# Kernel optimization log

Measured on AMD Instinct MI355X. Metric: run time of the kernel, lower is better.

The kernel has to match this reference:

```python
import jax, jax.numpy as jnp
import numpy as np
import math

N_HEADS = 16
DIM = 1024
D_HEAD = DIM // N_HEADS
BS, QLEN = 2, 2048


def setup_inputs() -> dict:
    key = jax.random.key(0)
    ks = jax.random.split(key, 10)
    s = 0.02
    return {
        "input": jax.random.normal(ks[0], (BS, QLEN, DIM), dtype=jnp.float32),
        "mask": jnp.ones((BS, QLEN), dtype=jnp.int32),
        "q_w": jax.random.normal(ks[1], (DIM, DIM), dtype=jnp.float32) * s,
        "q_b": jax.random.normal(ks[2], (DIM,), dtype=jnp.float32) * s,
        "k_w": jax.random.normal(ks[3], (DIM, DIM), dtype=jnp.float32) * s,
        "k_b": jax.random.normal(ks[4], (DIM,), dtype=jnp.float32) * s,
        "v_w": jax.random.normal(ks[5], (DIM, DIM), dtype=jnp.float32) * s,
        "v_b": jax.random.normal(ks[6], (DIM,), dtype=jnp.float32) * s,
        "o_w": jax.random.normal(ks[7], (DIM, DIM), dtype=jnp.float32) * s,
        "o_b": jax.random.normal(ks[8], (DIM,), dtype=jnp.float32) * s,
    }


def _shape(x, bs):
    # (bs, len, dim) -> (bs, heads, len, d_head)
    return x.reshape(bs, -1, N_HEADS, D_HEAD).transpose(0, 2, 1, 3)


def reference(input, mask, q_w, q_b, k_w, k_b, v_w, v_b, o_w, o_b):
    bs, qlen, dim = input.shape
    # projections (torch Linear: x @ W^T + b)
    q = _shape(input @ q_w.T + q_b, bs)
    k = _shape(input @ k_w.T + k_b, bs)
    v = _shape(input @ v_w.T + v_b, bs)
    q = q / math.sqrt(D_HEAD)
    # scores: (bs, heads, qlen, klen)
    scores = jnp.einsum("bhqd,bhkd->bhqk", q, k)
    pad = (mask == 0)[:, None, None, :]  # (bs,1,1,klen)
    scores = jnp.where(pad, -jnp.inf, scores)
    weights = jax.nn.softmax(scores.astype(jnp.float32), axis=-1).astype(scores.dtype)
    # dropout p=0.0 (eval) -> identity
    context = jnp.einsum("bhqk,bhkd->bhqd", weights, v)
    context = context.transpose(0, 2, 1, 3).reshape(bs, qlen, dim)
    return context @ o_w.T + o_b
```

## Files before the change

### kernel.cpp

```cpp
#include <hip/hip_runtime.h>


#define BS    2
#define QLEN  2048
#define DIM   1024
#define NH    16
#define DH    64
#define MTOK  (BS * QLEN)

#define QSCALE 0.18033688011112042f

typedef __attribute__((ext_vector_type(8))) short short8;
typedef __attribute__((ext_vector_type(4))) float float4_t;
typedef __attribute__((ext_vector_type(4))) int   int4_t;

__device__ __forceinline__ ushort f2bf(float f) {
    unsigned u = __float_as_uint(f);
    return (ushort)((u + 0x7fffu + ((u >> 16) & 1u)) >> 16);
}
__device__ __forceinline__ short8 pack8(float4 a0, float4 a1) {
    short8 r;
    r[0] = (short)f2bf(a0.x); r[1] = (short)f2bf(a0.y);
    r[2] = (short)f2bf(a0.z); r[3] = (short)f2bf(a0.w);
    r[4] = (short)f2bf(a1.x); r[5] = (short)f2bf(a1.y);
    r[6] = (short)f2bf(a1.z); r[7] = (short)f2bf(a1.w);
    return r;
}

__device__ __forceinline__ void glds16(const void* g, void* l) {
    __builtin_amdgcn_global_load_lds(
        (const __attribute__((address_space(1))) unsigned int*)g,
        (__attribute__((address_space(3))) unsigned int*)l, 16, 0, 0);
}

__global__ __launch_bounds__(256) void conv_all(
    const float* __restrict__ x,  const float* __restrict__ qw,
    const float* __restrict__ kw, const float* __restrict__ vw,
    const float* __restrict__ ow,
    ushort* __restrict__ Xbf, ushort* __restrict__ Wbf)
{
    const int blk = blockIdx.x;
    const float* s; ushort* d; size_t base;
    if (blk < 4096)      { s = x;  d = Xbf;             base = (size_t)blk * 1024; }
    else if (blk < 5120) { s = qw; d = Wbf;             base = (size_t)(blk - 4096) * 1024; }
    else if (blk < 6144) { s = kw; d = Wbf + 1048576;   base = (size_t)(blk - 5120) * 1024; }
    else if (blk < 7168) { s = vw; d = Wbf + 2097152;   base = (size_t)(blk - 6144) * 1024; }
    else                 { s = ow; d = Wbf + 3145728;   base = (size_t)(blk - 7168) * 1024; }
    const size_t i = base + threadIdx.x * 4;
    float4 v = *(const float4*)(s + i);
    ushort4 o;
    o.x = f2bf(v.x); o.y = f2bf(v.y); o.z = f2bf(v.z); o.w = f2bf(v.w);
    *(ushort4*)(d + i) = o;
}

__global__ __launch_bounds__(256) void transpose_v(
    const ushort* __restrict__ Vrow, ushort* __restrict__ Vt)
{
    __shared__ ushort T[64][72];
    const int tid  = threadIdx.x;
    const int tile = blockIdx.x;
    const int bh   = blockIdx.y;
    const int b = bh >> 4, h = bh & 15;

    #pragma unroll
    for (int rep = 0; rep < 2; ++rep) {
        int ch = tid + rep * 256;
        int tok = ch >> 3, seg = ch & 7;
        uint4 v = *(const uint4*)(Vrow + (size_t)(b * QLEN + tile * 64 + tok) * DIM
                                        + h * DH + seg * 8);
        *(uint4*)&T[tok][seg * 8] = v;
    }
    __syncthreads();
    #pragma unroll
    for (int rep = 0; rep < 2; ++rep) {
        int ch = tid + rep * 256;
        int dim = ch >> 3, tseg = ch & 7;
        ushort t0 = T[tseg * 8 + 0][dim], t1 = T[tseg * 8 + 1][dim];
        ushort t2 = T[tseg * 8 + 2][dim], t3 = T[tseg * 8 + 3][dim];
        ushort t4 = T[tseg * 8 + 4][dim], t5 = T[tseg * 8 + 5][dim];
        ushort t6 = T[tseg * 8 + 6][dim], t7 = T[tseg * 8 + 7][dim];
        uint4 o;
        o.x = (unsigned)t0 | ((unsigned)t1 << 16);
        o.y = (unsigned)t2 | ((unsigned)t3 << 16);
        o.z = (unsigned)t4 | ((unsigned)t5 << 16);
        o.w = (unsigned)t6 | ((unsigned)t7 << 16);
        *(uint4*)(Vt + (size_t)bh * DH * QLEN + (size_t)dim * QLEN
                      + tile * 64 + tseg * 8) = o;
    }
}

__global__ __launch_bounds__(256) void gemm_m97(
    const ushort* __restrict__ A, const ushort* __restrict__ Bw,
    const float* __restrict__ bias0, const float* __restrict__ bias1,
    const float* __restrict__ bias2,
    ushort* __restrict__ outQ, ushort* __restrict__ outK, ushort* __restrict__ outV,
    float* __restrict__ outF,
    int N, int K, int mode)
{
    __shared__ ushort As[128 * 32];
    __shared__ ushort Bs[128 * 32];
    const int tid  = threadIdx.x;
    const int w    = tid >> 6;
    const int lane = tid & 63;
    const int r15  = lane & 15;
    const int quad = lane >> 4;
    const int nblk = N >> 7;
    const int brow = blockIdx.x / nblk;
    const int bcol = blockIdx.x - brow * nblk;
    const int wrow = (w >> 1) * 64;
    const int wcol = (w & 1) * 64;

    float4_t acc[4][4];
    #pragma unroll
    for (int i = 0; i < 4; ++i)
        #pragma unroll
        for (int j = 0; j < 4; ++j)
            acc[i][j] = (float4_t){0.f, 0.f, 0.f, 0.f};

    int ch0 = w * 64 + lane;
    int ch1 = ch0 + 256;
    const int row0 = ch0 >> 2, s0 = ch0 & 3, gk0 = s0 ^ ((row0 >> 1) & 3);
    const int row1 = ch1 >> 2, s1 = ch1 & 3, gk1 = s1 ^ ((row1 >> 1) & 3);

    const ushort* ga0 = A + (size_t)(brow * 128 + row0) * K + gk0 * 8;
    const ushort* ga1 = A + (size_t)(brow * 128 + row1) * K + gk1 * 8;
    const ushort* gb0 = Bw + (size_t)(bcol * 128 + row0) * K + gk0 * 8;
    const ushort* gb1 = Bw + (size_t)(bcol * 128 + row1) * K + gk1 * 8;

    for (int k0 = 0; k0 < K; k0 += 32) {
        __syncthreads();
        glds16(ga0 + k0, As + ch0 * 8);
        glds16(ga1 + k0, As + ch1 * 8);
        glds16(gb0 + k0, Bs + ch0 * 8);
        glds16(gb1 + k0, Bs + ch1 * 8);
        __syncthreads();

        short8 af[4], bf[4];
        #pragma unroll
        for (int ms = 0; ms < 4; ++ms) {
            int row = wrow + ms * 16 + r15;
            int s = quad ^ ((row >> 1) & 3);
            af[ms] = *(const short8*)&As[row * 32 + s * 8];
        }
        #pragma unroll
        for (int ns = 0; ns < 4; ++ns) {
            int row = wcol + ns * 16 + r15;
            int s = quad ^ ((row >> 1) & 3);
            bf[ns] = *(const short8*)&Bs[row * 32 + s * 8];
        }
        #pragma unroll
        for (int ms = 0; ms < 4; ++ms)
            #pragma unroll
            for (int ns = 0; ns < 4; ++ns)
                acc[ms][ns] = __builtin_amdgcn_mfma_f32_16x16x32_bf16(
                    af[ms], bf[ns], acc[ms][ns], 0, 0, 0);
    }

    #pragma unroll
    for (int ms = 0; ms < 4; ++ms) {
        const int rowg = brow * 128 + wrow + ms * 16 + quad * 4;
        #pragma unroll
        for (int ns = 0; ns < 4; ++ns) {
            const int colg = bcol * 128 + wcol + ns * 16 + r15;
            if (mode == 0) {
                if (colg < 1024) {
                    const float bb = bias0[colg];
                    #pragma unroll
                    for (int r = 0; r < 4; ++r)
                        outQ[(size_t)(rowg + r) * 1024 + colg] =
                            f2bf((acc[ms][ns][r] + bb) * QSCALE);
                } else if (colg < 2048) {
                    const float bb = bias1[colg - 1024];
                    #pragma unroll
                    for (int r = 0; r < 4; ++r)
                        outK[(size_t)(rowg + r) * 1024 + (colg - 1024)] =
                            f2bf(acc[ms][ns][r] + bb);
                } else {
                    const float bb = bias2[colg - 2048];
                    #pragma unroll
                    for (int r = 0; r < 4; ++r)
                        outV[(size_t)(rowg + r) * 1024 + (colg - 2048)] =
                            f2bf(acc[ms][ns][r] + bb);
                }
            } else {
                const float bb = bias0[colg];
                #pragma unroll
                for (int r = 0; r < 4; ++r)
                    outF[(size_t)(rowg + r) * 1024 + colg] = acc[ms][ns][r] + bb;
            }
        }
    }
}

__global__ __launch_bounds__(256) void gemm_f32in_bf16out(
    const float* __restrict__ X, const float* __restrict__ W,
    const float* __restrict__ B, ushort* __restrict__ Out,
    int M, int N, int K, float scale)
{
    const int lane = threadIdx.x & 63;
    const int wid  = (blockIdx.x * blockDim.x + threadIdx.x) >> 6;
    const int tilesN = N >> 4;
    const int tm = wid / tilesN;
    const int tn = wid - tm * tilesN;
    const int r15  = lane & 15;
    const int quad = lane >> 4;

    const float* xp = X + (size_t)(tm * 16 + r15) * K + quad * 8;
    const float* wp = W + (size_t)(tn * 16 + r15) * K + quad * 8;

    float4_t acc = {0.f, 0.f, 0.f, 0.f};
    for (int k0 = 0; k0 < K; k0 += 32) {
        float4 a0 = *(const float4*)(xp + k0);
        float4 a1 = *(const float4*)(xp + k0 + 4);
        float4 b0 = *(const float4*)(wp + k0);
        float4 b1 = *(const float4*)(wp + k0 + 4);
        acc = __builtin_amdgcn_mfma_f32_16x16x32_bf16(pack8(a0, a1), pack8(b0, b1), acc, 0, 0, 0);
    }
    const int col  = tn * 16 + r15;
    const float bias = B[col];
    const int row0 = tm * 16 + quad * 4;
    #pragma unroll
    for (int r = 0; r < 4; ++r)
        Out[(size_t)(row0 + r) * N + col] = f2bf((acc[r] + bias) * scale);
}

__global__ __launch_bounds__(256) void gemm_bf16in_f32out(
    const ushort* __restrict__ X, const float* __restrict__ W,
    const float* __restrict__ B, float* __restrict__ Out,
    int M, int N, int K)
{
    const int lane = threadIdx.x & 63;
    const int wid  = (blockIdx.x * blockDim.x + threadIdx.x) >> 6;
    const int tilesN = N >> 4;
    const int tm = wid / tilesN;
    const int tn = wid - tm * tilesN;
    const int r15  = lane & 15;
    const int quad = lane >> 4;

    const ushort* xp = X + (size_t)(tm * 16 + r15) * K + quad * 8;
    const float*  wp = W + (size_t)(tn * 16 + r15) * K + quad * 8;

    float4_t acc = {0.f, 0.f, 0.f, 0.f};
    for (int k0 = 0; k0 < K; k0 += 32) {
        short8 a = *(const short8*)(xp + k0);
        float4 b0 = *(const float4*)(wp + k0);
        float4 b1 = *(const float4*)(wp + k0 + 4);
        acc = __builtin_amdgcn_mfma_f32_16x16x32_bf16(a, pack8(b0, b1), acc, 0, 0, 0);
    }
    const int col  = tn * 16 + r15;
    const float bias = B[col];
    const int row0 = tm * 16 + quad * 4;
    #pragma unroll
    for (int r = 0; r < 4; ++r)
        Out[(size_t)(row0 + r) * N + col] = acc[r] + bias;
}

__global__ __launch_bounds__(256) void flash_attn(
    const ushort* __restrict__ Qb, const ushort* __restrict__ Kb,
    const ushort* __restrict__ Vt, const int* __restrict__ mask,
    ushort* __restrict__ Cb)
{
    __shared__ __align__(16) ushort Ks[64][72];
    __shared__ __align__(16) ushort Vs[64][72];
    __shared__ __align__(16) float  Mb[QLEN];

    const int tid  = threadIdx.x;
    const int w    = tid >> 6;
    const int lane = tid & 63;
    const int r15  = lane & 15;
    const int quad = lane >> 4;
    const int bh = blockIdx.y;
    const int b = bh >> 4, h = bh & 15;

    {
        const int4* m4 = (const int4*)(mask + b * QLEN);
        #pragma unroll
        for (int rep = 0; rep < 2; ++rep) {
            const int idx = tid + rep * 256;
            int4 mv = m4[idx];
            float4 o;
            o.x = mv.x ? 0.f : -INFINITY;
            o.y = mv.y ? 0.f : -INFINITY;
            o.z = mv.z ? 0.f : -INFINITY;
            o.w = mv.w ? 0.f : -INFINITY;
            *(float4*)&Mb[idx * 4] = o;
        }
    }

    const int qbase = blockIdx.x * 128 + w * 32;
    const ushort* qp = Qb + (size_t)(b * QLEN + qbase + r15) * DIM + h * DH + quad * 8;
    short8 qf[2][2];
    qf[0][0] = *(const short8*)(qp);
    qf[0][1] = *(const short8*)(qp + 32);
    qf[1][0] = *(const short8*)(qp + 16 * DIM);
    qf[1][1] = *(const short8*)(qp + 16 * DIM + 32);

    const ushort* kg = Kb + (size_t)b * QLEN * DIM + h * DH;
    const ushort* vg = Vt + (size_t)bh * DH * QLEN;

    const int a0 = tid >> 3, seg = tid & 7;
    const int krow0 = (((a0 & 7) >> 2) << 4) + (((a0 >> 3) & 3) << 2) + (a0 & 3);

    float4_t o[2][4];
    #pragma unroll
    for (int rg = 0; rg < 2; ++rg)
        #pragma unroll
        for (int ds = 0; ds < 4; ++ds)
            o[rg][ds] = (float4_t){0.f, 0.f, 0.f, 0.f};
    float lp[2] = {0.f, 0.f};

    uint4 kr0, kr1, vr0, vr1;
    kr0 = *(const uint4*)(kg + (size_t)(a0     ) * DIM + seg * 8);
    kr1 = *(const uint4*)(kg + (size_t)(a0 + 32) * DIM + seg * 8);
    vr0 = *(const uint4*)(vg + (size_t)(a0     ) * QLEN + seg * 8);
    vr1 = *(const uint4*)(vg + (size_t)(a0 + 32) * QLEN + seg * 8);

    for (int kt = 0; kt < QLEN; kt += 64) {
        __syncthreads();
        *(uint4*)&Ks[krow0     ][seg * 8] = kr0;
        *(uint4*)&Ks[krow0 + 32][seg * 8] = kr1;
        *(uint4*)&Vs[a0        ][seg * 8] = vr0;
        *(uint4*)&Vs[a0 + 32   ][seg * 8] = vr1;
        __syncthreads();

        if (kt + 64 < QLEN) {
            kr0 = *(const uint4*)(kg + (size_t)(kt + 64 + a0     ) * DIM + seg * 8);
            kr1 = *(const uint4*)(kg + (size_t)(kt + 64 + a0 + 32) * DIM + seg * 8);
            vr0 = *(const uint4*)(vg + (size_t)(a0     ) * QLEN + kt + 64 + seg * 8);
            vr1 = *(const uint4*)(vg + (size_t)(a0 + 32) * QLEN + kt + 64 + seg * 8);
        }

        int pk[4][2][2];
        #pragma unroll
        for (int ks = 0; ks < 4; ++ks) {
            short8 kf0 = *(const short8*)&Ks[ks * 16 + r15][quad * 8];
            short8 kf1 = *(const short8*)&Ks[ks * 16 + r15][32 + quad * 8];
            const float4 mb = *(const float4*)&Mb[kt + ((ks >> 1) << 5)
                                                   + (quad << 3) + ((ks & 1) << 2)];
            #pragma unroll
            for (int rg = 0; rg < 2; ++rg) {
                float4_t s = {0.f, 0.f, 0.f, 0.f};
                s = __builtin_amdgcn_mfma_f32_16x16x32_bf16(kf0, qf[rg][0], s, 0, 0, 0);
                s = __builtin_amdgcn_mfma_f32_16x16x32_bf16(kf1, qf[rg][1], s, 0, 0, 0);
                unsigned u0 = __float_as_uint(exp2f(s[0] + mb.x));
                unsigned u1 = __float_as_uint(exp2f(s[1] + mb.y));
                unsigned u2 = __float_as_uint(exp2f(s[2] + mb.z));
                unsigned u3 = __float_as_uint(exp2f(s[3] + mb.w));
                lp[rg] += __uint_as_float(u0 & 0xffff0000u)
                        + __uint_as_float(u1 & 0xffff0000u)
                        + __uint_as_float(u2 & 0xffff0000u)
                        + __uint_as_float(u3 & 0xffff0000u);
                pk[ks][rg][0] = __builtin_amdgcn_perm(u1, u0, 0x07060302);
                pk[ks][rg][1] = __builtin_amdgcn_perm(u3, u2, 0x07060302);
            }
        }

        #pragma unroll
        for (int ck = 0; ck < 2; ++ck) {
            short8 vf[4];
            #pragma unroll
            for (int ds = 0; ds < 4; ++ds)
                vf[ds] = *(const short8*)&Vs[ds * 16 + r15][ck * 32 + quad * 8];
            #pragma unroll
            for (int rg = 0; rg < 2; ++rg) {
                int4_t pfi = { pk[2 * ck][rg][0], pk[2 * ck][rg][1],
                               pk[2 * ck + 1][rg][0], pk[2 * ck + 1][rg][1] };
                short8 pf = __builtin_bit_cast(short8, pfi);
                #pragma unroll
                for (int ds = 0; ds < 4; ++ds)
                    o[rg][ds] = __builtin_amdgcn_mfma_f32_16x16x32_bf16(
                        pf, vf[ds], o[rg][ds], 0, 0, 0);
            }
        }
    }

    #pragma unroll
    for (int rg = 0; rg < 2; ++rg) {
        float l = lp[rg];
        l += __shfl_xor(l, 16, 64);
        l += __shfl_xor(l, 32, 64);
        const float inv = 1.f / fmaxf(l, 1e-30f);
        #pragma unroll
        for (int r = 0; r < 4; ++r) {
            const float ir = __shfl(inv, quad * 4 + r, 64);
            const size_t rb = (size_t)(b * QLEN + qbase + rg * 16 + quad * 4 + r) * DIM
                              + h * DH;
            Cb[rb +  0 + r15] = f2bf(o[rg][0][r] * ir);
            Cb[rb + 16 + r15] = f2bf(o[rg][1][r] * ir);
            Cb[rb + 32 + r15] = f2bf(o[rg][2][r] * ir);
            Cb[rb + 48 + r15] = f2bf(o[rg][3][r] * ir);
        }
    }
}

extern "C" void kernel_launch(void* const* d_in, const int* in_sizes, int n_in,
                              void* d_out, int out_size, void* d_ws, size_t ws_size,
                              hipStream_t stream)
{
    const float* x    = (const float*)d_in[0];
    const int*   mask = (const int*)d_in[1];
    const float* q_w  = (const float*)d_in[2];
    const float* q_b  = (const float*)d_in[3];
    const float* k_w  = (const float*)d_in[4];
    const float* k_b  = (const float*)d_in[5];
    const float* v_w  = (const float*)d_in[6];
    const float* v_b  = (const float*)d_in[7];
    const float* o_w  = (const float*)d_in[8];
    const float* o_b  = (const float*)d_in[9];
    float* out = (float*)d_out;

    const size_t SEG = (size_t)MTOK * DIM;
    ushort* Qbf = (ushort*)d_out;
    ushort* Xbf = Qbf + SEG;
    ushort* Kb  = (ushort*)d_ws;
    ushort* Vrow = Kb + SEG;
    ushort* Cb   = Vrow;
    ushort* Vt  = Vrow + SEG;
    ushort* Wbf = Vt + SEG;

    const bool big = ws_size >= (size_t)32 * 1024 * 1024;

    if (big) {
        conv_all<<<8192, 256, 0, stream>>>(x, q_w, k_w, v_w, o_w, Xbf, Wbf);
        gemm_m97<<<(MTOK / 128) * (3072 / 128), 256, 0, stream>>>(
            Xbf, Wbf, q_b, k_b, v_b, Qbf, Kb, Vrow, nullptr, 3072, DIM, 0);
    } else {
        const int tiles   = (MTOK / 16) * (DIM / 16);
        const int gblocks = tiles / 4;
        gemm_f32in_bf16out<<<gblocks, 256, 0, stream>>>(x, q_w, q_b, Qbf, MTOK, DIM, DIM, QSCALE);
        gemm_f32in_bf16out<<<gblocks, 256, 0, stream>>>(x, k_w, k_b, Kb,  MTOK, DIM, DIM, 1.0f);
        gemm_f32in_bf16out<<<gblocks, 256, 0, stream>>>(x, v_w, v_b, Vrow, MTOK, DIM, DIM, 1.0f);
    }

    transpose_v<<<dim3(QLEN / 64, BS * NH), 256, 0, stream>>>(Vrow, Vt);

    flash_attn<<<dim3(QLEN / 128, BS * NH), 256, 0, stream>>>(Qbf, Kb, Vt, mask, Cb);

    if (big) {
        gemm_m97<<<(MTOK / 128) * (DIM / 128), 256, 0, stream>>>(
            Cb, Wbf + 3 * (size_t)(DIM * DIM), o_b, nullptr, nullptr,
            nullptr, nullptr, nullptr, out, DIM, DIM, 1);
    } else {
        const int tiles = (MTOK / 16) * (DIM / 16);
        gemm_bf16in_f32out<<<tiles / 4, 256, 0, stream>>>(Cb, o_w, o_b, out, MTOK, DIM, DIM);
    }
}
```

Measured before the change: 226.3 us.

## Double-buffer K/V LDS tiles with XOR swizzle and MFMA-based row sums

Replaces the single padded K/V shared tiles with double-buffered, XOR-swizzled unpadded tiles. The next tile is written to the alternate buffer after compute, so each iteration needs one barrier instead of two. The softmax denominator now comes from an extra MFMA against a ones vector instead of scalar adds and shuffles. exp2f is also replaced by the hardware exp2 intrinsic. This costs extra LDS for the second buffer and extra MFMA issue, and the swizzle indexing has to match the fragment layout exactly.

```diff
diff --git a/kernel.cpp b/kernel.cpp
--- a/kernel.cpp
+++ b/kernel.cpp
@@ -260,8 +260,8 @@
     const ushort* __restrict__ Vt, const int* __restrict__ mask,
     ushort* __restrict__ Cb)
 {
-    __shared__ __align__(16) ushort Ks[64][72];
-    __shared__ __align__(16) ushort Vs[64][72];
+    __shared__ __align__(16) ushort Ks[2][64][64];
+    __shared__ __align__(16) ushort Vs[2][64][64];
     __shared__ __align__(16) float  Mb[QLEN];
 
     const int tid  = threadIdx.x;
@@ -300,30 +300,37 @@
 
     const int a0 = tid >> 3, seg = tid & 7;
     const int krow0 = (((a0 & 7) >> 2) << 4) + (((a0 >> 3) & 3) << 2) + (a0 & 3);
+    const int sK = (seg ^ (krow0 & 7)) << 3;
+    const int sV = (seg ^ (a0 & 7)) << 3;
+    const int xq = (quad ^ (r15 & 7)) << 3;
 
     float4_t o[2][4];
-    #pragma unroll
-    for (int rg = 0; rg < 2; ++rg)
+    float4_t ol[2];
+    #pragma unroll
+    for (int rg = 0; rg < 2; ++rg) {
+        ol[rg] = (float4_t){0.f, 0.f, 0.f, 0.f};
         #pragma unroll
         for (int ds = 0; ds < 4; ++ds)
             o[rg][ds] = (float4_t){0.f, 0.f, 0.f, 0.f};
-    float lp[2] = {0.f, 0.f};
-
-    uint4 kr0, kr1, vr0, vr1;
-    kr0 = *(const uint4*)(kg + (size_t)(a0     ) * DIM + seg * 8);
-    kr1 = *(const uint4*)(kg + (size_t)(a0 + 32) * DIM + seg * 8);
-    vr0 = *(const uint4*)(vg + (size_t)(a0     ) * QLEN + seg * 8);
-    vr1 = *(const uint4*)(vg + (size_t)(a0 + 32) * QLEN + seg * 8);
-
+    }
+    short8 ones8;
+    #pragma unroll
+    for (int i = 0; i < 8; ++i) ones8[i] = (short)0x3F80;
+
+    uint4 kr0 = *(const uint4*)(kg + (size_t)(a0     ) * DIM + seg * 8);
+    uint4 kr1 = *(const uint4*)(kg + (size_t)(a0 + 32) * DIM + seg * 8);
+    uint4 vr0 = *(const uint4*)(vg + (size_t)(a0     ) * QLEN + seg * 8);
+    uint4 vr1 = *(const uint4*)(vg + (size_t)(a0 + 32) * QLEN + seg * 8);
+    *(uint4*)&Ks[0][krow0     ][sK] = kr0;
+    *(uint4*)&Ks[0][krow0 + 32][sK] = kr1;
+    *(uint4*)&Vs[0][a0        ][sV] = vr0;
+    *(uint4*)&Vs[0][a0 + 32   ][sV] = vr1;
+    __syncthreads();
+
+    int p = 0;
     for (int kt = 0; kt < QLEN; kt += 64) {
-        __syncthreads();
-        *(uint4*)&Ks[krow0     ][seg * 8] = kr0;
-        *(uint4*)&Ks[krow0 + 32][seg * 8] = kr1;
-        *(uint4*)&Vs[a0        ][seg * 8] = vr0;
-        *(uint4*)&Vs[a0 + 32   ][seg * 8] = vr1;
-        __syncthreads();
-
-        if (kt + 64 < QLEN) {
+        const bool more = (kt + 64 < QLEN);
+        if (more) {
             kr0 = *(const uint4*)(kg + (size_t)(kt + 64 + a0     ) * DIM + seg * 8);
             kr1 = *(const uint4*)(kg + (size_t)(kt + 64 + a0 + 32) * DIM + seg * 8);
             vr0 = *(const uint4*)(vg + (size_t)(a0     ) * QLEN + kt + 64 + seg * 8);
@@ -333,8 +340,9 @@
         int pk[4][2][2];
         #pragma unroll
         for (int ks = 0; ks < 4; ++ks) {
-            short8 kf0 = *(const short8*)&Ks[ks * 16 + r15][quad * 8];
-            short8 kf1 = *(const short8*)&Ks[ks * 16 + r15][32 + quad * 8];
+            const ushort* krow = &Ks[p][ks * 16 + r15][0];
+            short8 kf0 = *(const short8*)(krow + xq);
+            short8 kf1 = *(const short8*)(krow + (xq ^ 32));
             const float4 mb = *(const float4*)&Mb[kt + ((ks >> 1) << 5)
                                                    + (quad << 3) + ((ks & 1) << 2)];
             #pragma unroll
@@ -342,14 +350,10 @@
                 float4_t s = {0.f, 0.f, 0.f, 0.f};
                 s = __builtin_amdgcn_mfma_f32_16x16x32_bf16(kf0, qf[rg][0], s, 0, 0, 0);
                 s = __builtin_amdgcn_mfma_f32_16x16x32_bf16(kf1, qf[rg][1], s, 0, 0, 0);
-                unsigned u0 = __float_as_uint(exp2f(s[0] + mb.x));
-                unsigned u1 = __float_as_uint(exp2f(s[1] + mb.y));
-                unsigned u2 = __float_as_uint(exp2f(s[2] + mb.z));
-                unsigned u3 = __float_as_uint(exp2f(s[3] + mb.w));
-                lp[rg] += __uint_as_float(u0 & 0xffff0000u)
-                        + __uint_as_float(u1 & 0xffff0000u)
-                        + __uint_as_float(u2 & 0xffff0000u)
-                        + __uint_as_float(u3 & 0xffff0000u);
+                unsigned u0 = __float_as_uint(__builtin_amdgcn_exp2f(s[0] + mb.x));
+                unsigned u1 = __float_as_uint(__builtin_amdgcn_exp2f(s[1] + mb.y));
+                unsigned u2 = __float_as_uint(__builtin_amdgcn_exp2f(s[2] + mb.z));
+                unsigned u3 = __float_as_uint(__builtin_amdgcn_exp2f(s[3] + mb.w));
                 pk[ks][rg][0] = __builtin_amdgcn_perm(u1, u0, 0x07060302);
                 pk[ks][rg][1] = __builtin_amdgcn_perm(u3, u2, 0x07060302);
             }
@@ -360,7 +364,7 @@
             short8 vf[4];
             #pragma unroll
             for (int ds = 0; ds < 4; ++ds)
-                vf[ds] = *(const short8*)&Vs[ds * 16 + r15][ck * 32 + quad * 8];
+                vf[ds] = *(const short8*)(&Vs[p][ds * 16 + r15][0] + (xq ^ (ck << 5)));
             #pragma unroll
             for (int rg = 0; rg < 2; ++rg) {
                 int4_t pfi = { pk[2 * ck][rg][0], pk[2 * ck][rg][1],
@@ -370,19 +374,26 @@
                 for (int ds = 0; ds < 4; ++ds)
                     o[rg][ds] = __builtin_amdgcn_mfma_f32_16x16x32_bf16(
                         pf, vf[ds], o[rg][ds], 0, 0, 0);
+                ol[rg] = __builtin_amdgcn_mfma_f32_16x16x32_bf16(
+                    pf, ones8, ol[rg], 0, 0, 0);
             }
         }
+
+        if (more) {
+            *(uint4*)&Ks[p ^ 1][krow0     ][sK] = kr0;
+            *(uint4*)&Ks[p ^ 1][krow0 + 32][sK] = kr1;
+            *(uint4*)&Vs[p ^ 1][a0        ][sV] = vr0;
+            *(uint4*)&Vs[p ^ 1][a0 + 32   ][sV] = vr1;
+        }
+        __syncthreads();
+        p ^= 1;
     }
 
     #pragma unroll
     for (int rg = 0; rg < 2; ++rg) {
-        float l = lp[rg];
-        l += __shfl_xor(l, 16, 64);
-        l += __shfl_xor(l, 32, 64);
-        const float inv = 1.f / fmaxf(l, 1e-30f);
         #pragma unroll
         for (int r = 0; r < 4; ++r) {
-            const float ir = __shfl(inv, quad * 4 + r, 64);
+            const float ir = 1.f / fmaxf(ol[rg][r], 1e-30f);
             const size_t rb = (size_t)(b * QLEN + qbase + rg * 16 + quad * 4 + r) * DIM
                               + h * DH;
             Cb[rb +  0 + r15] = f2bf(o[rg][0][r] * ir);
```

Result: faster. 210.3 us (-7.1%).
